# Performance work log

Hardware: AMD Instinct MI355X
Metric: run time of the kernel (lower is better)

## Reference

```python
import jax, jax.numpy as jnp
import numpy as np

B, LV, HW, LT, D, H = 4, 16, 196, 32, 768, 12
DH = D // H
SCALE = 1.0 / np.sqrt(DH).astype(np.float32)


def _lin(x, W, b):
    # torch nn.Linear convention: W is [out, in]
    return x @ W.T + b


def _split_heads(x):
    # (..., D) -> (..., H, DH)
    return x.reshape(*x.shape[:-1], H, DH)


def _attn_logits(feat_q, feat_k, mask_q, mask_k, Wq, bq, Wk, bk):
    # feat_q: (B, LV, Lq, D), feat_k: (B, LV, Lk, D)
    q = _split_heads(_lin(feat_q, Wq, bq))  # b v q h d
    k = _split_heads(_lin(feat_k, Wk, bk))  # b v k h d
    logits = jnp.einsum('bvqhd,bvkhd->bvhqk', q, k)
    m = (mask_q[:, :, None] & mask_k[:, None, :])[:, None, None]  # b 1 1 q k
    return jnp.where(m, logits, -10000.0)


def setup_inputs() -> dict:
    key = jax.random.key(0)
    ks = jax.random.split(key, 12)
    inp = {
        'vid_feat': jax.random.normal(ks[0], (B, LV, HW, D), jnp.float32),
        'txt_feat': jax.random.normal(ks[1], (B, LV, LT, D), jnp.float32),
        'vid_mask': jnp.ones((B, LV), dtype=bool),
        'txt_mask': jax.random.randint(ks[2], (B, LT), 0, 2) > 0,
    }
    for i, name in enumerate(['v2v', 't2v', 't2t', 'v2t']):
        inp[name + '_W'] = jax.random.normal(ks[3 + 2 * i], (3, D, D), jnp.float32) * 0.02
        inp[name + '_b'] = jnp.zeros((3, D), jnp.float32)
    return inp


def reference(vid_feat, txt_feat, vid_mask, txt_mask,
              v2v_W, v2v_b, t2v_W, t2v_b, t2t_W, t2t_b, v2t_W, v2t_b):
    mask_hw = jnp.ones((vid_feat.shape[0], HW), dtype=bool)

    # values: concat video-keys then text-keys along the key axis
    v_value = jnp.concatenate([_lin(vid_feat, v2v_W[2], v2v_b[2]),
                               _lin(txt_feat, t2v_W[2], t2v_b[2])], axis=2)
    v_value = _split_heads(v_value)  # b v (HW+LT) h d
    t_value = jnp.concatenate([_lin(vid_feat, v2t_W[2], v2t_b[2]),
                               _lin(txt_feat, t2t_W[2], t2t_b[2])], axis=2)
    t_value = _split_heads(t_value)

    # logits (source call order: get_attn_logits(feat_k, mask_k, feat_q, mask_q, ...))
    v2v = _attn_logits(vid_feat, vid_feat, mask_hw, mask_hw, v2v_W[0], v2v_b[0], v2v_W[1], v2v_b[1])
    t2v = _attn_logits(vid_feat, txt_feat, mask_hw, txt_mask, t2v_W[0], t2v_b[0], t2v_W[1], t2v_b[1])
    v2t = _attn_logits(txt_feat, vid_feat, txt_mask, mask_hw, v2t_W[0], v2t_b[0], v2t_W[1], v2t_b[1])
    t2t = _attn_logits(txt_feat, txt_feat, txt_mask, txt_mask, t2t_W[0], t2t_b[0], t2t_W[1], t2t_b[1])

    v_logits = jnp.concatenate([v2v, t2v], axis=-1)  # b v h HW (HW+LT)
    t_logits = jnp.concatenate([v2t, t2t], axis=-1)  # b v h LT (HW+LT)

    # NOTE: source scales probabilities AFTER softmax by 1/sqrt(d_head)
    vid_out = jnp.einsum('bvhqk,bvkhd->bvqhd', jax.nn.softmax(v_logits, axis=-1) * SCALE, v_value)
    vid_out = vid_out.reshape(*vid_out.shape[:3], D)
    txt_out = jnp.einsum('bvhqk,bvkhd->bvqhd', jax.nn.softmax(t_logits, axis=-1) * SCALE, t_value)
    txt_out = txt_out.reshape(*txt_out.shape[:3], D)
    return (vid_out, txt_out)
```

## Files before the change

kernel.cpp:

```cpp
#include <hip/hip_runtime.h>

#define NBV 64
#define HWN 196
#define LTN 32
#define DIM 768
#define NH 12
#define DHD 64
#define ATT_SCALE 0.125f

typedef __attribute__((ext_vector_type(8))) __bf16 bf16x8;
typedef __attribute__((ext_vector_type(4))) float f32x4;

static __device__ __forceinline__ unsigned short f2bf(float f) {
    union { float f; unsigned u; } v; v.f = f;
    unsigned r = v.u + 0x7FFFu + ((v.u >> 16) & 1u);
    return (unsigned short)(r >> 16);
}

#define MFMA16(a, b, c) __builtin_amdgcn_mfma_f32_16x16x32_bf16((a), (b), (c), 0, 0, 0)
#define GLOAD_LDS16(g, l)                                                      \
    __builtin_amdgcn_global_load_lds(                                          \
        (const __attribute__((address_space(1))) void*)(g),                    \
        (__attribute__((address_space(3))) void*)(l), 16, 0, 0)

__device__ __forceinline__ void compute_tile(const unsigned short* sa,
                                             const unsigned short* sb,
                                             f32x4 (&acc)[8][4])
{
    bf16x8 af[8], bg[4];
#pragma unroll
    for (int m = 0; m < 4; ++m) af[m] = *(const bf16x8*)(sa + m * 512);
#pragma unroll
    for (int n = 0; n < 4; ++n) bg[n] = *(const bf16x8*)(sb + n * 512);
#pragma unroll
    for (int m = 4; m < 8; ++m) af[m] = *(const bf16x8*)(sa + m * 512);
    __builtin_amdgcn_s_setprio(1);
#pragma unroll
    for (int m = 0; m < 4; ++m)
#pragma unroll
        for (int n = 0; n < 4; ++n)
            acc[m][n] = MFMA16(bg[n], af[m], acc[m][n]);
    __builtin_amdgcn_s_setprio(0);
    __builtin_amdgcn_s_setprio(1);
#pragma unroll
    for (int m = 4; m < 8; ++m)
#pragma unroll
        for (int n = 0; n < 4; ++n)
            acc[m][n] = MFMA16(bg[n], af[m], acc[m][n]);
    __builtin_amdgcn_s_setprio(0);
}

struct CvtCfg {
    const float* src[14];
    unsigned short* dst[14];
    int n4[14];
};

__global__ __launch_bounds__(256) void cvt_bf16(CvtCfg cfg) {
    const int e = blockIdx.y;
    const float4* s = (const float4*)cfg.src[e];
    unsigned short* d = cfg.dst[e];
    const int n4 = cfg.n4[e];
    for (int i = blockIdx.x * 256 + threadIdx.x; i < n4; i += gridDim.x * 256) {
        float4 v = s[i];
        ushort4 o;
        o.x = f2bf(v.x); o.y = f2bf(v.y); o.z = f2bf(v.z); o.w = f2bf(v.w);
        *(ushort4*)(d + (long)i * 4) = o;
    }
}

struct GemmCfg {
    const unsigned short* A[2];
    const unsigned short* W[2];
    unsigned short* out[2];
    const float* bias[2][6];
    int M[2];
};

__global__ __launch_bounds__(512, 2) void gemm_proj(GemmCfg cfg, int nb0)
{
    __shared__ __align__(16) unsigned short lds[65536];
    const int tid = threadIdx.x;
    const int lane = tid & 63, wid = tid >> 6;
    const int wm = wid >> 2, wn = wid & 3;
    const int fr = lane & 15, fg = lane >> 4;

    const int nwg = gridDim.x;
    const int orig = blockIdx.x;
    const int q = nwg >> 3, r = nwg & 7;
    const int xcd = orig & 7, lid = orig >> 3;
    const int wg = (xcd < r ? xcd * (q + 1) : r * (q + 1) + (xcd - r) * q) + lid;

    const int set = wg >= nb0;
    const int local = wg - (set ? nb0 : 0);
    const int mt = local / 18, nt = local - mt * 18;
    const int m0 = mt * 256, n0 = nt * 256;
    const int M = cfg.M[set];
    const unsigned short* __restrict__ A = cfg.A[set];
    const unsigned short* __restrict__ W = cfg.W[set];

    const int srow = tid >> 2;
    const int sxor = ((tid & 3) ^ ((tid >> 3) & 3)) * 8;
    const unsigned short* aSrc = A + (long)(m0 + srow) * DIM + sxor;
    const unsigned short* bSrc = W + (long)(n0 + srow) * DIM + sxor;
    unsigned short* ldst = lds + tid * 8;

    const int rxor = (fg ^ ((fr >> 1) & 3)) * 8;
    const int aoff = (wm * 128 + fr) * 32 + rxor;
    const int boff = 8192 + (wn * 64 + fr) * 32 + rxor;

    f32x4 acc[8][4] = {};

#define STAGE(t, s) do {                                                       \
    const unsigned short* _a = aSrc + (t) * 32;                                \
    const unsigned short* _b = bSrc + (t) * 32;                                \
    unsigned short* _d = ldst + (s) * 16384;                                   \
    GLOAD_LDS16(_a, _d);                                                       \
    GLOAD_LDS16(_a + 98304, _d + 4096);                                        \
    GLOAD_LDS16(_b, _d + 8192);                                                \
    GLOAD_LDS16(_b + 98304, _d + 12288);                                       \
} while (0)

    STAGE(0, 0); STAGE(1, 1); STAGE(2, 2);
#pragma unroll 1
    for (int t = 0; t < 21; ++t) {
        asm volatile("s_waitcnt vmcnt(8)" ::: "memory");
        __builtin_amdgcn_s_barrier();
        STAGE(t + 3, (t + 3) & 3);
        {
            const unsigned short* base = lds + (t & 3) * 16384;
            compute_tile(base + aoff, base + boff, acc);
        }
    }
    asm volatile("s_waitcnt vmcnt(8)" ::: "memory");
    __builtin_amdgcn_s_barrier();
    { const unsigned short* base = lds + 16384;     compute_tile(base + aoff, base + boff, acc); }
    asm volatile("s_waitcnt vmcnt(4)" ::: "memory");
    __builtin_amdgcn_s_barrier();
    { const unsigned short* base = lds + 2 * 16384; compute_tile(base + aoff, base + boff, acc); }
    asm volatile("s_waitcnt vmcnt(0)" ::: "memory");
    __builtin_amdgcn_s_barrier();
    { const unsigned short* base = lds + 3 * 16384; compute_tile(base + aoff, base + boff, acc); }

#undef STAGE

    const int w = nt / 3;
    const int nlb = (nt - w * 3) * 256;
    const float* bp = cfg.bias[set][w];
    unsigned short* op = cfg.out[set] + (long)w * M * DIM;
    const int colL = wn * 64;
    asm volatile("" ::: "memory");
    __builtin_amdgcn_s_barrier();
#pragma unroll
    for (int p = 0; p < 2; ++p) {
        if (wm == p) {
#pragma unroll
            for (int n = 0; n < 4; ++n) {
                float4 b4 = *(const float4*)(bp + nlb + colL + n * 16 + fg * 4);
#pragma unroll
                for (int m = 0; m < 8; ++m) {
                    ushort4 u;
                    u.x = f2bf(acc[m][n][0] + b4.x);
                    u.y = f2bf(acc[m][n][1] + b4.y);
                    u.z = f2bf(acc[m][n][2] + b4.z);
                    u.w = f2bf(acc[m][n][3] + b4.w);
                    *(ushort4*)&lds[(m * 16 + fr) * 264 + colL + n * 16 + fg * 4] = u;
                }
            }
        }
        __builtin_amdgcn_s_barrier();
#pragma unroll
        for (int i = 0; i < 8; ++i) {
            int chunk = tid + i * 512;
            int rr = chunk >> 5, cb = chunk & 31;
            bf16x8 v = *(const bf16x8*)&lds[rr * 264 + cb * 8];
            *(bf16x8*)(op + (long)(m0 + p * 128 + rr) * DIM + nlb + cb * 8) = v;
        }
        if (p == 0) __builtin_amdgcn_s_barrier();
    }
}

struct TransCfg {
    const unsigned short* src[4];
    unsigned short* dst[4];
};

__global__ __launch_bounds__(256) void transpose_v(TransCfg cfg)
{
    __shared__ unsigned short t[32][33];
    const int x = blockIdx.x;
    const int which = x >> 3;
    const int xi = x & 7;
    const int istxt = (xi == 7);
    const unsigned short* src = cfg.src[which * 2 + istxt];
    unsigned short* dst = cfg.dst[which];
    const int nrows = istxt ? LTN : HWN;
    const int colbase = istxt ? 208 : 0;
    const int rt = istxt ? 0 : xi;

    const int bv = blockIdx.z, dt = blockIdx.y;
    const int tx = threadIdx.x & 31, ty = threadIdx.x >> 5;
#pragma unroll
    for (int i = 0; i < 4; ++i) {
        int r = rt * 32 + ty + i * 8;
        t[ty + i * 8][tx] = (r < nrows)
            ? src[(long)(bv * nrows + r) * DIM + dt * 32 + tx] : (unsigned short)0;
    }
    __syncthreads();
#pragma unroll
    for (int i = 0; i < 4; ++i) {
        int d = dt * 32 + ty + i * 8;
        int rr = rt * 32 + tx;
        if (rr < nrows)
            dst[(long)(bv * DIM + d) * 256 + colbase + rr] = t[tx][ty + i * 8];
    }
}

struct AttnCfg {
    const unsigned short* QA[2];
    const unsigned short* QB[2];
    const unsigned short* KV[2];
    const unsigned short* KT[2];
    const unsigned short* Vt[2];
    float* outp[2];
};

__global__ __launch_bounds__(256, 2) void attn_kernel(AttnCfg cfg,
                                                      const int* __restrict__ tmask)
{
    __shared__ __align__(16) unsigned short P[4][16][264];
    const int tid = threadIdx.x, lane = tid & 63, wid = tid >> 6;
    const int bv = blockIdx.x, h = blockIdx.y;
    const int b = bv >> 4;
    const int sel = (blockIdx.z == 4);
    const int nq = sel ? LTN : HWN;
    const unsigned short* QA = cfg.QA[sel];
    const unsigned short* QB = cfg.QB[sel];
    const unsigned short* KV = cfg.KV[sel];
    const unsigned short* KT = cfg.KT[sel];
    const unsigned short* Vt = cfg.Vt[sel];
    float* outp = cfg.outp[sel];
    const int q0 = (sel ? 0 : blockIdx.z * 64) + wid * 16;
    const int fr = lane & 15, fg = lane >> 4;

    if (q0 >= ((nq + 15) & ~15)) return;

    int qr = q0 + fr; if (qr > nq - 1) qr = nq - 1;
    const unsigned short* qa_p = QA + (long)(bv * nq + qr) * DIM + h * DHD;
    const unsigned short* qb_p = QB + (long)(bv * nq + qr) * DIM + h * DHD;
    bf16x8 qa[2], qb[2];
#pragma unroll
    for (int kh = 0; kh < 2; ++kh) {
        qa[kh] = *(const bf16x8*)(qa_p + kh * 32 + fg * 8);
        qb[kh] = *(const bf16x8*)(qb_p + kh * 32 + fg * 8);
    }

    f32x4 acc[15];
#pragma unroll
    for (int kb = 0; kb < 13; ++kb) {
        int kr = kb * 16 + fr; if (kr > HWN - 1) kr = HWN - 1;
        const unsigned short* kp = KV + (long)(bv * HWN + kr) * DIM + h * DHD;
        f32x4 c = {0.f, 0.f, 0.f, 0.f};
        c = MFMA16(*(const bf16x8*)(kp + fg * 8), qa[0], c);
        c = MFMA16(*(const bf16x8*)(kp + 32 + fg * 8), qa[1], c);
        acc[kb] = c;
    }
#pragma unroll
    for (int kb = 13; kb < 15; ++kb) {
        int kr = (kb - 13) * 16 + fr;
        const unsigned short* kp = KT + (long)(bv * LTN + kr) * DIM + h * DHD;
        f32x4 c = {0.f, 0.f, 0.f, 0.f};
        c = MFMA16(*(const bf16x8*)(kp + fg * 8), qb[0], c);
        c = MFMA16(*(const bf16x8*)(kp + 32 + fg * 8), qb[1], c);
        acc[kb] = c;
    }

    int tm = tmask[b * LTN + (lane & 31)];
    bool vq = true;
    if (sel) {
        int qi = q0 + fr; if (qi > LTN - 1) qi = LTN - 1;
        vq = __shfl(tm, qi, 64) != 0;
    }
#pragma unroll
    for (int kb = 0; kb < 15; ++kb) {
#pragma unroll
        for (int j = 0; j < 4; ++j) {
            int c = kb * 16 + fg * 4 + j;
            bool kreal = (c < HWN) || (c >= 208);
            bool kvalid = true;
            if (c >= 208) kvalid = __shfl(tm, c - 208, 64) != 0;
            float l = acc[kb][j];
            if (!kreal) l = -3.0e38f;
            else if (!(kvalid && vq)) l = -10000.0f;
            acc[kb][j] = l;
        }
    }

    float mx = -3.0e38f;
#pragma unroll
    for (int kb = 0; kb < 15; ++kb)
#pragma unroll
        for (int j = 0; j < 4; ++j) mx = fmaxf(mx, acc[kb][j]);
    mx = fmaxf(mx, __shfl_xor(mx, 16, 64));
    mx = fmaxf(mx, __shfl_xor(mx, 32, 64));
    float s = 0.f;
#pragma unroll
    for (int kb = 0; kb < 15; ++kb)
#pragma unroll
        for (int j = 0; j < 4; ++j) {
            float p = __expf(acc[kb][j] - mx);
            acc[kb][j] = p;
            s += p;
        }
    s += __shfl_xor(s, 16, 64);
    s += __shfl_xor(s, 32, 64);

    unsigned short* pw = &P[wid][fr][0];
#pragma unroll
    for (int kb = 0; kb < 15; ++kb) {
        ushort4 u;
        u.x = f2bf(acc[kb][0]); u.y = f2bf(acc[kb][1]);
        u.z = f2bf(acc[kb][2]); u.w = f2bf(acc[kb][3]);
        *(ushort4*)(pw + kb * 16 + fg * 4) = u;
    }
    {
        ushort4 z = {0, 0, 0, 0};
        *(ushort4*)(pw + 240 + fg * 4) = z;
    }

    f32x4 oacc[4] = {};
    const unsigned short* vt_base = Vt + ((long)bv * DIM + h * DHD) * 256;
#pragma unroll
    for (int ks = 0; ks < 8; ++ks) {
        bf16x8 pf = *(const bf16x8*)(pw + ks * 32 + fg * 8);
#pragma unroll
        for (int n = 0; n < 4; ++n) {
            const unsigned short* vp = vt_base + (long)(n * 16 + fr) * 256 + ks * 32 + fg * 8;
            oacc[n] = MFMA16(*(const bf16x8*)vp, pf, oacc[n]);
        }
    }

    if (q0 + fr < nq) {
        float inv = ATT_SCALE / s;
        float* ob = outp + (long)(bv * nq + q0 + fr) * DIM + h * DHD;
#pragma unroll
        for (int n = 0; n < 4; ++n) {
            float4 o;
            o.x = oacc[n][0] * inv; o.y = oacc[n][1] * inv;
            o.z = oacc[n][2] * inv; o.w = oacc[n][3] * inv;
            *(float4*)(ob + n * 16 + fg * 4) = o;
        }
    }
}

extern "C" void kernel_launch(void* const* d_in, const int* in_sizes, int n_in,
                              void* d_out, int out_size, void* d_ws, size_t ws_size,
                              hipStream_t stream)
{
    const float* vid_feat = (const float*)d_in[0];
    const float* txt_feat = (const float*)d_in[1];
    const int*   txt_mask = (const int*)d_in[3];
    const float* v2v_W = (const float*)d_in[4];
    const float* v2v_b = (const float*)d_in[5];
    const float* t2v_W = (const float*)d_in[6];
    const float* t2v_b = (const float*)d_in[7];
    const float* t2t_W = (const float*)d_in[8];
    const float* t2t_b = (const float*)d_in[9];
    const float* v2t_W = (const float*)d_in[10];
    const float* v2t_b = (const float*)d_in[11];

    char* ws = (char*)d_ws;
    unsigned short* vid_bf   = (unsigned short*)(ws);
    unsigned short* txt_bf   = (unsigned short*)(ws + 19267584L);
    unsigned short* Wv_bf    = (unsigned short*)(ws + 22413312L);
    unsigned short* Wt_bf    = (unsigned short*)(ws + 29491200L);
    unsigned short* proj_vid = (unsigned short*)(ws + 36569088L);
    unsigned short* proj_txt = (unsigned short*)(ws + 152174592L);
    unsigned short* Vt_v     = (unsigned short*)(ws + 171048960L);
    unsigned short* Vt_t     = (unsigned short*)(ws + 196214784L);

    const long WSL = 589824;
    CvtCfg cc;
    cc.src[0] = vid_feat; cc.dst[0] = vid_bf; cc.n4[0] = 9633792 / 4;
    cc.src[1] = txt_feat; cc.dst[1] = txt_bf; cc.n4[1] = 1572864 / 4;
    const float* wsrc_v[6] = { v2v_W, v2v_W + WSL, t2v_W, v2t_W + WSL,
                               v2v_W + 2 * WSL, v2t_W + 2 * WSL };
    const float* wsrc_t[6] = { t2v_W + WSL, t2v_W + 2 * WSL, v2t_W, t2t_W,
                               t2t_W + WSL, t2t_W + 2 * WSL };
    for (int i = 0; i < 6; ++i) {
        cc.src[2 + i] = wsrc_v[i]; cc.dst[2 + i] = Wv_bf + (long)i * WSL; cc.n4[2 + i] = WSL / 4;
        cc.src[8 + i] = wsrc_t[i]; cc.dst[8 + i] = Wt_bf + (long)i * WSL; cc.n4[8 + i] = WSL / 4;
    }
    cvt_bf16<<<dim3(2048, 14), 256, 0, stream>>>(cc);

    GemmCfg gc;
    gc.A[0] = vid_bf;  gc.W[0] = Wv_bf;  gc.out[0] = proj_vid;  gc.M[0] = 12544;
    gc.A[1] = txt_bf;  gc.W[1] = Wt_bf;  gc.out[1] = proj_txt;  gc.M[1] = 2048;
    const float* bsrc_v[6] = { v2v_b, v2v_b + 768, t2v_b, v2t_b + 768,
                               v2v_b + 1536, v2t_b + 1536 };
    const float* bsrc_t[6] = { t2v_b + 768, t2v_b + 1536, v2t_b, t2t_b,
                               t2t_b + 768, t2t_b + 1536 };
    for (int i = 0; i < 6; ++i) { gc.bias[0][i] = bsrc_v[i]; gc.bias[1][i] = bsrc_t[i]; }
    gemm_proj<<<dim3(49 * 18 + 8 * 18), 512, 0, stream>>>(gc, 49 * 18);

    const long PV = 12544L * 768, PT = 2048L * 768;
    TransCfg tc;
    tc.src[0] = proj_vid + 4 * PV;  tc.src[1] = proj_txt + 1 * PT;  tc.dst[0] = Vt_v;
    tc.src[2] = proj_vid + 5 * PV;  tc.src[3] = proj_txt + 5 * PT;  tc.dst[1] = Vt_t;
    transpose_v<<<dim3(16, 24, 64), 256, 0, stream>>>(tc);

    float* out_f = (float*)d_out;
    AttnCfg ac;
    ac.QA[0] = proj_vid + 0 * PV;  ac.QB[0] = proj_vid + 2 * PV;
    ac.KV[0] = proj_vid + 1 * PV;  ac.KT[0] = proj_txt + 0 * PT;
    ac.Vt[0] = Vt_v;               ac.outp[0] = out_f;
    ac.QA[1] = proj_txt + 2 * PT;  ac.QB[1] = proj_txt + 3 * PT;
    ac.KV[1] = proj_vid + 3 * PV;  ac.KT[1] = proj_txt + 4 * PT;
    ac.Vt[1] = Vt_t;               ac.outp[1] = out_f + 9633792;
    attn_kernel<<<dim3(64, 12, 5), 256, 0, stream>>>(ac, txt_mask);
}
```

Before: 271.9 us.

## Rebalance grids for convert, transpose and attention kernels

```diff
diff --git a/kernel.cpp b/kernel.cpp
--- a/kernel.cpp
+++ b/kernel.cpp
@@ -53,20 +53,19 @@
 struct CvtCfg {
     const float* src[14];
     unsigned short* dst[14];
-    int n4[14];
+    int start[14];
 };
 
 __global__ __launch_bounds__(256) void cvt_bf16(CvtCfg cfg) {
-    const int e = blockIdx.y;
-    const float4* s = (const float4*)cfg.src[e];
-    unsigned short* d = cfg.dst[e];
-    const int n4 = cfg.n4[e];
-    for (int i = blockIdx.x * 256 + threadIdx.x; i < n4; i += gridDim.x * 256) {
-        float4 v = s[i];
-        ushort4 o;
-        o.x = f2bf(v.x); o.y = f2bf(v.y); o.z = f2bf(v.z); o.w = f2bf(v.w);
-        *(ushort4*)(d + (long)i * 4) = o;
-    }
+    const int b = blockIdx.x;
+    int e = 0;
+#pragma unroll
+    for (int k = 1; k < 14; ++k) e += (b >= cfg.start[k]);
+    const long i = (long)(b - cfg.start[e]) * 256 + threadIdx.x;
+    float4 v = ((const float4*)cfg.src[e])[i];
+    ushort4 o;
+    o.x = f2bf(v.x); o.y = f2bf(v.y); o.z = f2bf(v.z); o.w = f2bf(v.w);
+    *(ushort4*)(cfg.dst[e] + i * 4) = o;
 }
 
 struct GemmCfg {
@@ -198,21 +197,25 @@
     const int colbase = istxt ? 208 : 0;
     const int rt = istxt ? 0 : xi;
 
-    const int bv = blockIdx.z, dt = blockIdx.y;
+    const int bv = blockIdx.z;
     const int tx = threadIdx.x & 31, ty = threadIdx.x >> 5;
-#pragma unroll
-    for (int i = 0; i < 4; ++i) {
-        int r = rt * 32 + ty + i * 8;
-        t[ty + i * 8][tx] = (r < nrows)
-            ? src[(long)(bv * nrows + r) * DIM + dt * 32 + tx] : (unsigned short)0;
-    }
-    __syncthreads();
-#pragma unroll
-    for (int i = 0; i < 4; ++i) {
-        int d = dt * 32 + ty + i * 8;
-        int rr = rt * 32 + tx;
-        if (rr < nrows)
-            dst[(long)(bv * DIM + d) * 256 + colbase + rr] = t[tx][ty + i * 8];
+    for (int it = 0; it < 4; ++it) {
+        const int dt = blockIdx.y * 4 + it;
+#pragma unroll
+        for (int i = 0; i < 4; ++i) {
+            int r = rt * 32 + ty + i * 8;
+            t[ty + i * 8][tx] = (r < nrows)
+                ? src[(long)(bv * nrows + r) * DIM + dt * 32 + tx] : (unsigned short)0;
+        }
+        __syncthreads();
+#pragma unroll
+        for (int i = 0; i < 4; ++i) {
+            int d = dt * 32 + ty + i * 8;
+            int rr = rt * 32 + tx;
+            if (rr < nrows)
+                dst[(long)(bv * DIM + d) * 256 + colbase + rr] = t[tx][ty + i * 8];
+        }
+        __syncthreads();
     }
 }
 
@@ -225,14 +228,25 @@
     float* outp[2];
 };
 
-__global__ __launch_bounds__(256, 2) void attn_kernel(AttnCfg cfg,
+__global__ __launch_bounds__(256, 3) void attn_kernel(AttnCfg cfg,
                                                       const int* __restrict__ tmask)
 {
     __shared__ __align__(16) unsigned short P[4][16][264];
     const int tid = threadIdx.x, lane = tid & 63, wid = tid >> 6;
     const int bv = blockIdx.x, h = blockIdx.y;
     const int b = bv >> 4;
-    const int sel = (blockIdx.z == 4);
+    const int zz = blockIdx.z;
+
+    int sel, q0;
+    if (zz < 3) {
+        sel = 0;
+        q0 = zz * 64 + wid * 16;
+    } else {
+        if (wid == 3) return;
+        sel = (wid >= 1);
+        q0 = sel ? (wid - 1) * 16 : 192;
+    }
+
     const int nq = sel ? LTN : HWN;
     const unsigned short* QA = cfg.QA[sel];
     const unsigned short* QB = cfg.QB[sel];
@@ -240,10 +254,7 @@
     const unsigned short* KT = cfg.KT[sel];
     const unsigned short* Vt = cfg.Vt[sel];
     float* outp = cfg.outp[sel];
-    const int q0 = (sel ? 0 : blockIdx.z * 64) + wid * 16;
     const int fr = lane & 15, fg = lane >> 4;
-
-    if (q0 >= ((nq + 15) & ~15)) return;
 
     int qr = q0 + fr; if (qr > nq - 1) qr = nq - 1;
     const unsigned short* qa_p = QA + (long)(bv * nq + qr) * DIM + h * DHD;
@@ -381,17 +392,24 @@
 
     const long WSL = 589824;
     CvtCfg cc;
-    cc.src[0] = vid_feat; cc.dst[0] = vid_bf; cc.n4[0] = 9633792 / 4;
-    cc.src[1] = txt_feat; cc.dst[1] = txt_bf; cc.n4[1] = 1572864 / 4;
+    cc.src[0] = vid_feat; cc.dst[0] = vid_bf;
+    cc.src[1] = txt_feat; cc.dst[1] = txt_bf;
     const float* wsrc_v[6] = { v2v_W, v2v_W + WSL, t2v_W, v2t_W + WSL,
                                v2v_W + 2 * WSL, v2t_W + 2 * WSL };
     const float* wsrc_t[6] = { t2v_W + WSL, t2v_W + 2 * WSL, v2t_W, t2t_W,
                                t2t_W + WSL, t2t_W + 2 * WSL };
     for (int i = 0; i < 6; ++i) {
-        cc.src[2 + i] = wsrc_v[i]; cc.dst[2 + i] = Wv_bf + (long)i * WSL; cc.n4[2 + i] = WSL / 4;
-        cc.src[8 + i] = wsrc_t[i]; cc.dst[8 + i] = Wt_bf + (long)i * WSL; cc.n4[8 + i] = WSL / 4;
-    }
-    cvt_bf16<<<dim3(2048, 14), 256, 0, stream>>>(cc);
+        cc.src[2 + i] = wsrc_v[i]; cc.dst[2 + i] = Wv_bf + (long)i * WSL;
+        cc.src[8 + i] = wsrc_t[i]; cc.dst[8 + i] = Wt_bf + (long)i * WSL;
+    }
+    {
+        int st = 0;
+        int nb[14];
+        nb[0] = 9408; nb[1] = 1536;
+        for (int i = 2; i < 14; ++i) nb[i] = 576;
+        for (int i = 0; i < 14; ++i) { cc.start[i] = st; st += nb[i]; }
+        cvt_bf16<<<dim3(st), 256, 0, stream>>>(cc);
+    }
 
     GemmCfg gc;
     gc.A[0] = vid_bf;  gc.W[0] = Wv_bf;  gc.out[0] = proj_vid;  gc.M[0] = 12544;
@@ -407,7 +425,7 @@
     TransCfg tc;
     tc.src[0] = proj_vid + 4 * PV;  tc.src[1] = proj_txt + 1 * PT;  tc.dst[0] = Vt_v;
     tc.src[2] = proj_vid + 5 * PV;  tc.src[3] = proj_txt + 5 * PT;  tc.dst[1] = Vt_t;
-    transpose_v<<<dim3(16, 24, 64), 256, 0, stream>>>(tc);
+    transpose_v<<<dim3(16, 6, 64), 256, 0, stream>>>(tc);
 
     float* out_f = (float*)d_out;
     AttnCfg ac;
@@ -417,5 +435,5 @@
     ac.QA[1] = proj_txt + 2 * PT;  ac.QB[1] = proj_txt + 3 * PT;
     ac.KV[1] = proj_vid + 3 * PV;  ac.KT[1] = proj_txt + 4 * PT;
     ac.Vt[1] = Vt_t;               ac.outp[1] = out_f + 9633792;
-    attn_kernel<<<dim3(64, 12, 5), 256, 0, stream>>>(ac, txt_mask);
-}
+    attn_kernel<<<dim3(64, 12, 4), 256, 0, stream>>>(ac, txt_mask);
+}
```

After: 279.9 us. 2.9% more time.
